# Performance work log

Hardware: AMD Instinct MI355X
Metric: run time of the kernel (lower is better)

Reference implementation:

```python
import jax, jax.numpy as jnp
import numpy as np

NUM_HEADS = 16
HEAD_DIM = 64
Q_DIM = K_DIM = V_DIM = 1024
LQ = LK = 4096
TAU = HEAD_DIM ** (-0.5)


def setup_inputs() -> dict:
    key = jax.random.key(0)
    ks = jax.random.split(key, 11)
    inner = NUM_HEADS * HEAD_DIM
    s = 0.02
    return {
        "q": jax.random.normal(ks[0], (LQ, Q_DIM), dtype=jnp.float32),
        "k": jax.random.normal(ks[1], (LK, K_DIM), dtype=jnp.float32),
        "v": jax.random.normal(ks[2], (LK, V_DIM), dtype=jnp.float32),
        "Wq": jax.random.normal(ks[3], (Q_DIM, inner), dtype=jnp.float32) * s,
        "bq": jax.random.normal(ks[4], (inner,), dtype=jnp.float32) * s,
        "Wk": jax.random.normal(ks[5], (K_DIM, inner), dtype=jnp.float32) * s,
        "bk": jax.random.normal(ks[6], (inner,), dtype=jnp.float32) * s,
        "Wv": jax.random.normal(ks[7], (V_DIM, inner), dtype=jnp.float32) * s,
        "bv": jax.random.normal(ks[8], (inner,), dtype=jnp.float32) * s,
        "Wo": jax.random.normal(ks[9], (inner, Q_DIM), dtype=jnp.float32) * s,
        "bo": jax.random.normal(ks[10], (Q_DIM,), dtype=jnp.float32) * s,
    }


def reference(q, k, v, Wq, bq, Wk, bk, Wv, bv, Wo, bo):
    h, x = NUM_HEADS, HEAD_DIM
    # projections: [L, h*x] -> per-head layout
    qh = (q @ Wq + bq).reshape(-1, h, x)  # [Lq, h, x]
    kh = (k @ Wk + bk).reshape(-1, h, x)  # [Lk, h, x]
    vh = (v @ Wv + bv).reshape(-1, h, x)  # [Lk, h, x]
    # scores: [h, Lq, Lk]
    att = jnp.einsum('qhx,khx->hqk', qh, kh) * TAU
    att = jax.nn.softmax(att, axis=-1)  # dropout=0.0 -> identity
    ctx = jnp.einsum('hqk,khx->qhx', att, vh).reshape(-1, h * x)  # [Lq, h*x]
    out = ctx @ Wo + bo  # [Lq, Q_DIM]
    return out, att
```

## Files before the change

kernel.cpp:

```cpp
#include <hip/hip_runtime.h>
#include <hip/hip_bf16.h>

typedef unsigned short ushort_t;
typedef __attribute__((ext_vector_type(8))) short short8;
typedef __attribute__((ext_vector_type(8))) __bf16 bf16x8;
typedef __attribute__((ext_vector_type(4))) float f32x4;

#define LQS 4096
#define LKS 4096
#define NH 16
#define HD 64
#define DIN 1024
#define QBLK 64
#define KVB 64
static constexpr float TAU_S = 0.125f;
static constexpr float LOG2E = 1.4426950408889634f;

__device__ __forceinline__ float exp2_fast(float x) { return __builtin_amdgcn_exp2f(x); }

__device__ __forceinline__ ushort_t f32_to_bf16(float x) {
  union { float f; unsigned u; } v; v.f = x;
  unsigned r = v.u + 0x7FFF + ((v.u >> 16) & 1);
  return (ushort_t)(r >> 16);
}

__device__ __forceinline__ void gld_lds16(const void* g, void* l) {
  __builtin_amdgcn_global_load_lds((const __attribute__((address_space(1))) void*)g,
                                   (__attribute__((address_space(3))) void*)l, 16, 0, 0);
}

__device__ __forceinline__ f32x4 mfma16(bf16x8 a, bf16x8 b, f32x4 c) {
  return __builtin_amdgcn_mfma_f32_16x16x32_bf16(a, b, c, 0, 0, 0);
}

struct Cvt3 { const float* src[3]; ushort_t* dst[3]; };
__global__ void cvt_kernel(Cvt3 c) {
  const float* __restrict__ src = c.src[blockIdx.y];
  ushort_t* __restrict__ dst = c.dst[blockIdx.y];
  int i = (blockIdx.x * 256 + threadIdx.x) * 8;
  float4 a = *(const float4*)(src + i);
  float4 b = *(const float4*)(src + i + 4);
  short8 o;
  o[0] = (short)f32_to_bf16(a.x); o[1] = (short)f32_to_bf16(a.y);
  o[2] = (short)f32_to_bf16(a.z); o[3] = (short)f32_to_bf16(a.w);
  o[4] = (short)f32_to_bf16(b.x); o[5] = (short)f32_to_bf16(b.y);
  o[6] = (short)f32_to_bf16(b.z); o[7] = (short)f32_to_bf16(b.w);
  *(short8*)(dst + i) = o;
}

struct TW4 { const float* W[4]; ushort_t* Wt[4]; };
__global__ void transpose_w(TW4 w) {
  const float* __restrict__ W = w.W[blockIdx.z];
  ushort_t* __restrict__ Wt = w.Wt[blockIdx.z];
  __shared__ float tile[64][65];
  const int t = threadIdx.x;
  const int k0 = blockIdx.y * 64, n0 = blockIdx.x * 64;
#pragma unroll
  for (int i = 0; i < 16; ++i) {
    int idx = i * 256 + t;
    int r = idx >> 6, c = idx & 63;
    tile[r][c] = W[(size_t)(k0 + r) * DIN + n0 + c];
  }
  __syncthreads();
#pragma unroll
  for (int i = 0; i < 16; ++i) {
    int idx = i * 256 + t;
    int r = idx >> 6, c = idx & 63;
    Wt[(size_t)(n0 + r) * DIN + k0 + c] = f32_to_bf16(tile[c][r]);
  }
}

__global__ void transpose_v(const ushort_t* __restrict__ vh, ushort_t* __restrict__ vt) {
  __shared__ ushort_t tile[64][65];
  const int t = threadIdx.x;
  const int k0 = blockIdx.x * 64, h = blockIdx.y;
#pragma unroll
  for (int i = 0; i < 16; ++i) {
    int idx = i * 256 + t;
    int r = idx >> 6, c = idx & 63;
    tile[r][c] = vh[(size_t)(k0 + r) * DIN + h * HD + c];
  }
  __syncthreads();
#pragma unroll
  for (int i = 0; i < 16; ++i) {
    int idx = i * 256 + t;
    int r = idx >> 6, c = idx & 63;
    vt[((size_t)h * HD + r) * (size_t)LKS + k0 + c] = tile[c][r];
  }
}

struct Batch3 {
  const ushort_t* A[3];
  const ushort_t* Bt[3];
  const float* bias[3];
  void* C[3];
  float scale[3];
};
template <bool OUT_F32>
__launch_bounds__(256, 2)
__global__ void gemm_nt(Batch3 bt3) {
  const int bid = blockIdx.x;
  const int xcd = bid & 7, idx = bid >> 3;
  const int z = idx >> 5, rem = idx & 31;
  const int by = xcd * 4 + (rem >> 3), bx = rem & 7;
  const ushort_t* __restrict__ A = bt3.A[z];
  const ushort_t* __restrict__ Bt = bt3.Bt[z];
  const float* __restrict__ bias = bt3.bias[z];
  void* __restrict__ Cout = bt3.C[z];
  const float scale = bt3.scale[z];
  const int K = DIN, N = DIN;

  __shared__ __align__(16) ushort_t Alds[128 * 64];
  __shared__ __align__(16) ushort_t Blds[128 * 64];
  const int t = threadIdx.x, wave = t >> 6, lane = t & 63;
  const int l15 = lane & 15, lg = lane >> 4;
  const int m0 = by * 128, n0 = bx * 128;
  const int wr = wave >> 1, wc = wave & 1;
  f32x4 acc[4][4];
#pragma unroll
  for (int i = 0; i < 4; ++i)
#pragma unroll
    for (int j = 0; j < 4; ++j) acc[i][j] = (f32x4){0.f, 0.f, 0.f, 0.f};

  for (int tk = 0; tk < K / 64; ++tk) {
#pragma unroll
    for (int c = 0; c < 4; ++c) {
      int chunk = wave * 4 + c;
      int row = chunk * 8 + (lane >> 3);
      int ss = (lane & 7) ^ (row & 7);
      gld_lds16(A + (size_t)(m0 + row) * K + tk * 64 + ss * 8, (char*)Alds + chunk * 1024);
      gld_lds16(Bt + (size_t)(n0 + row) * K + tk * 64 + ss * 8, (char*)Blds + chunk * 1024);
    }
    __syncthreads();
#pragma unroll
    for (int kk = 0; kk < 2; ++kk) {
      bf16x8 a[4], b[4];
#pragma unroll
      for (int i = 0; i < 4; ++i) {
        int ra = wr * 64 + i * 16 + l15;
        a[i] = *(const bf16x8*)((const char*)Alds + ra * 128 + ((((kk * 4 + lg) << 4)) ^ ((ra & 7) << 4)));
        int rb = wc * 64 + i * 16 + l15;
        b[i] = *(const bf16x8*)((const char*)Blds + rb * 128 + ((((kk * 4 + lg) << 4)) ^ ((rb & 7) << 4)));
      }
#pragma unroll
      for (int mi = 0; mi < 4; ++mi)
#pragma unroll
        for (int ni = 0; ni < 4; ++ni)
          acc[mi][ni] = mfma16(a[mi], b[ni], acc[mi][ni]);
    }
    __syncthreads();
  }
#pragma unroll
  for (int ni = 0; ni < 4; ++ni) {
    int coln = n0 + wc * 64 + ni * 16 + l15;
    float bv = bias[coln];
#pragma unroll
    for (int mi = 0; mi < 4; ++mi) {
#pragma unroll
      for (int r = 0; r < 4; ++r) {
        int rowm = m0 + wr * 64 + mi * 16 + lg * 4 + r;
        float v = (acc[mi][ni][r] + bv) * scale;
        if (OUT_F32)
          ((float*)Cout)[(size_t)rowm * N + coln] = v;
        else
          ((ushort_t*)Cout)[(size_t)rowm * N + coln] = f32_to_bf16(v);
      }
    }
  }
}

__launch_bounds__(256, 4)
__global__ void attn_kernel(const ushort_t* __restrict__ qh, const ushort_t* __restrict__ kh,
                            const ushort_t* __restrict__ vt, float* __restrict__ att,
                            ushort_t* __restrict__ ctx) {
  __shared__ __align__(16) ushort_t Klds[KVB * 64];
  __shared__ __align__(16) ushort_t Vlds[KVB * 64];
  __shared__ __align__(16) float Patt[4][16 * 64];
  const int t = threadIdx.x, wave = t >> 6, lane = t & 63;
  const int l15 = lane & 15, lg = lane >> 4;
  const int bid = blockIdx.x;
  const int xcd = bid & 7, idx = bid >> 3;
  const int h = xcd * 2 + (idx >> 6);
  const int q0 = (idx & 63) * QBLK;

  char* Pw = (char*)Patt[wave];

  bf16x8 qa[2];
  {
    int row = q0 + wave * 16 + l15;
    const ushort_t* qp = qh + (size_t)row * DIN + h * HD + lg * 8;
    qa[0] = *(const bf16x8*)(qp);
    qa[1] = *(const bf16x8*)(qp + 32);
  }

  const int srow8 = lane >> 3;
  const int sslot = (lane & 7);

  float rs[4] = {0.f, 0.f, 0.f, 0.f};
  for (int tk = 0; tk < LKS / KVB; ++tk) {
#pragma unroll
    for (int c = 0; c < 2; ++c) {
      int chunk = wave * 2 + c;
      int row = chunk * 8 + srow8;
      int ss = sslot ^ (row & 7);
      gld_lds16(kh + (size_t)(tk * KVB + row) * DIN + h * HD + ss * 8, (char*)Klds + chunk * 1024);
    }
    __syncthreads();
#pragma unroll
    for (int ct = 0; ct < 4; ++ct) {
      f32x4 acc = (f32x4){0.f, 0.f, 0.f, 0.f};
#pragma unroll
      for (int kk = 0; kk < 2; ++kk) {
        int row = ct * 16 + l15;
        bf16x8 kb = *(const bf16x8*)((const char*)Klds + row * 128 + ((((kk * 4 + lg) << 4)) ^ ((row & 7) << 4)));
        acc = mfma16(qa[kk], kb, acc);
      }
#pragma unroll
      for (int r = 0; r < 4; ++r) rs[r] += exp2_fast(acc[r]);
    }
    __syncthreads();
  }
#pragma unroll
  for (int m = 1; m < 16; m <<= 1) {
#pragma unroll
    for (int r = 0; r < 4; ++r) rs[r] += __shfl_xor(rs[r], m, 64);
  }
  float recip[4];
#pragma unroll
  for (int r = 0; r < 4; ++r) recip[r] = 1.0f / rs[r];

  f32x4 cacc[4];
#pragma unroll
  for (int x = 0; x < 4; ++x) cacc[x] = (f32x4){0.f, 0.f, 0.f, 0.f};
  float* atth = att + ((size_t)h << 24);

  for (int tk = 0; tk < LKS / KVB; ++tk) {
#pragma unroll
    for (int c = 0; c < 2; ++c) {
      int chunk = wave * 2 + c;
      int row = chunk * 8 + srow8;
      int ss = sslot ^ (row & 7);
      gld_lds16(kh + (size_t)(tk * KVB + row) * DIN + h * HD + ss * 8, (char*)Klds + chunk * 1024);
      gld_lds16(vt + ((size_t)h * HD + row) * (size_t)LKS + tk * KVB + ss * 8, (char*)Vlds + chunk * 1024);
    }
    __syncthreads();
#pragma unroll
    for (int ct = 0; ct < 4; ++ct) {
      f32x4 acc = (f32x4){0.f, 0.f, 0.f, 0.f};
#pragma unroll
      for (int kk = 0; kk < 2; ++kk) {
        int row = ct * 16 + l15;
        bf16x8 kb = *(const bf16x8*)((const char*)Klds + row * 128 + ((((kk * 4 + lg) << 4)) ^ ((row & 7) << 4)));
        acc = mfma16(qa[kk], kb, acc);
      }
#pragma unroll
      for (int r = 0; r < 4; ++r) {
        float p = exp2_fast(acc[r]) * recip[r];
        int R = lg * 4 + r;
        int col = ct * 16 + l15;
        int slot = col >> 2;
        *(float*)(Pw + R * 256 + (((slot ^ R)) << 4) + (col & 3) * 4) = p;
      }
    }
#pragma unroll
    for (int i = 0; i < 4; ++i) {
      int slot = lg + 4 * i;
      f32x4 v = *(const f32x4*)(Pw + l15 * 256 + ((slot ^ l15) << 4));
      int rowq = q0 + wave * 16 + l15;
      *(f32x4*)(atth + (((size_t)rowq) << 12) + tk * KVB + slot * 4) = v;
    }
    bf16x8 pa[2];
#pragma unroll
    for (int kk = 0; kk < 2; ++kk) {
      int s0 = kk * 8 + lg * 2;
      f32x4 lo = *(const f32x4*)(Pw + l15 * 256 + ((s0 ^ l15) << 4));
      f32x4 hi = *(const f32x4*)(Pw + l15 * 256 + (((s0 + 1) ^ l15) << 4));
      short8 sp;
#pragma unroll
      for (int j = 0; j < 4; ++j) {
        sp[j] = (short)f32_to_bf16(lo[j]);
        sp[4 + j] = (short)f32_to_bf16(hi[j]);
      }
      pa[kk] = *(bf16x8*)&sp;
    }
#pragma unroll
    for (int x = 0; x < 4; ++x) {
#pragma unroll
      for (int kk = 0; kk < 2; ++kk) {
        int rv = x * 16 + l15;
        bf16x8 vb = *(const bf16x8*)((const char*)Vlds + rv * 128 + ((((kk * 4 + lg) << 4)) ^ ((rv & 7) << 4)));
        cacc[x] = mfma16(pa[kk], vb, cacc[x]);
      }
    }
    __syncthreads();
  }
#pragma unroll
  for (int x = 0; x < 4; ++x) {
#pragma unroll
    for (int r = 0; r < 4; ++r) {
      int rowq = q0 + wave * 16 + lg * 4 + r;
      int col = h * HD + x * 16 + l15;
      ctx[(size_t)rowq * DIN + col] = f32_to_bf16(cacc[x][r]);
    }
  }
}

extern "C" void kernel_launch(void* const* d_in, const int* in_sizes, int n_in,
                              void* d_out, int out_size, void* d_ws, size_t ws_size,
                              hipStream_t stream) {
  const float* q = (const float*)d_in[0];
  const float* k = (const float*)d_in[1];
  const float* v = (const float*)d_in[2];
  const float* Wq = (const float*)d_in[3];
  const float* bq = (const float*)d_in[4];
  const float* Wk = (const float*)d_in[5];
  const float* bk = (const float*)d_in[6];
  const float* Wv = (const float*)d_in[7];
  const float* bv = (const float*)d_in[8];
  const float* Wo = (const float*)d_in[9];
  const float* bo = (const float*)d_in[10];

  float* out = (float*)d_out;
  float* att = out + (size_t)LQS * DIN;

  char* ws = (char*)d_ws;
  ushort_t* qhb = (ushort_t*)(ws + (size_t)0);
  ushort_t* khb = (ushort_t*)(ws + ((size_t)8 << 20));
  ushort_t* vhb = (ushort_t*)(ws + ((size_t)16 << 20));
  ushort_t* vtb = (ushort_t*)(ws + ((size_t)24 << 20));
  ushort_t* ctx = (ushort_t*)(ws + ((size_t)32 << 20));
  ushort_t* qb = (ushort_t*)(ws + ((size_t)40 << 20));
  ushort_t* kb = (ushort_t*)(ws + ((size_t)48 << 20));
  ushort_t* vb = (ushort_t*)(ws + ((size_t)56 << 20));
  ushort_t* Wqt = (ushort_t*)(ws + ((size_t)64 << 20));
  ushort_t* Wkt = (ushort_t*)(ws + ((size_t)66 << 20));
  ushort_t* Wvt = (ushort_t*)(ws + ((size_t)68 << 20));
  ushort_t* Wot = (ushort_t*)(ws + ((size_t)70 << 20));

  Cvt3 c3;
  c3.src[0] = q; c3.src[1] = k; c3.src[2] = v;
  c3.dst[0] = qb; c3.dst[1] = kb; c3.dst[2] = vb;
  cvt_kernel<<<dim3(LQS * DIN / 8 / 256, 3), 256, 0, stream>>>(c3);

  TW4 w4;
  w4.W[0] = Wq; w4.W[1] = Wk; w4.W[2] = Wv; w4.W[3] = Wo;
  w4.Wt[0] = Wqt; w4.Wt[1] = Wkt; w4.Wt[2] = Wvt; w4.Wt[3] = Wot;
  transpose_w<<<dim3(16, 16, 4), 256, 0, stream>>>(w4);

  Batch3 pb;
  pb.A[0] = qb; pb.A[1] = kb; pb.A[2] = vb;
  pb.Bt[0] = Wqt; pb.Bt[1] = Wkt; pb.Bt[2] = Wvt;
  pb.bias[0] = bq; pb.bias[1] = bk; pb.bias[2] = bv;
  pb.C[0] = qhb; pb.C[1] = khb; pb.C[2] = vhb;
  pb.scale[0] = TAU_S * LOG2E; pb.scale[1] = 1.0f; pb.scale[2] = 1.0f;
  gemm_nt<false><<<768, 256, 0, stream>>>(pb);

  transpose_v<<<dim3(64, 16), 256, 0, stream>>>(vhb, vtb);

  attn_kernel<<<1024, 256, 0, stream>>>(qhb, khb, vtb, att, ctx);

  Batch3 ob;
  ob.A[0] = ctx; ob.A[1] = ctx; ob.A[2] = ctx;
  ob.Bt[0] = Wot; ob.Bt[1] = Wot; ob.Bt[2] = Wot;
  ob.bias[0] = bo; ob.bias[1] = bo; ob.bias[2] = bo;
  ob.C[0] = out; ob.C[1] = out; ob.C[2] = out;
  ob.scale[0] = 1.0f; ob.scale[1] = 1.0f; ob.scale[2] = 1.0f;
  gemm_nt<true><<<256, 256, 0, stream>>>(ob);
}
```

Baseline: 451.9 us.

## Transpose QK^T MFMA to keep P in registers and drop LDS staging

Swaps the MFMA operand order so each lane holds a row of scores for one query, letting the probability tile be written to global memory and fed to the PV MFMA directly from registers instead of passing through an LDS staging buffer. The row-sum reduction is shortened to two shuffles, and normalization folds log2 of the sum into the exponent, removing a multiply per element. V operand fetches are rebuilt from two 8-byte LDS reads to match the new P register layout. This removes LDS write/read traffic for P and frees shared memory, but adds split V loads that may raise LDS instruction count.

After: 434.7 us. 1.04x faster.

```diff
diff --git a/kernel.cpp b/kernel.cpp
--- a/kernel.cpp
+++ b/kernel.cpp
@@ -17,6 +17,7 @@
 static constexpr float LOG2E = 1.4426950408889634f;
 
 __device__ __forceinline__ float exp2_fast(float x) { return __builtin_amdgcn_exp2f(x); }
+__device__ __forceinline__ float log2_fast(float x) { return __builtin_amdgcn_logf(x); }
 
 __device__ __forceinline__ ushort_t f32_to_bf16(float x) {
   union { float f; unsigned u; } v; v.f = x;
@@ -175,20 +176,17 @@
                             ushort_t* __restrict__ ctx) {
   __shared__ __align__(16) ushort_t Klds[KVB * 64];
   __shared__ __align__(16) ushort_t Vlds[KVB * 64];
-  __shared__ __align__(16) float Patt[4][16 * 64];
   const int t = threadIdx.x, wave = t >> 6, lane = t & 63;
   const int l15 = lane & 15, lg = lane >> 4;
   const int bid = blockIdx.x;
   const int xcd = bid & 7, idx = bid >> 3;
   const int h = xcd * 2 + (idx >> 6);
   const int q0 = (idx & 63) * QBLK;
-
-  char* Pw = (char*)Patt[wave];
+  const int w0 = q0 + wave * 16;
 
   bf16x8 qa[2];
   {
-    int row = q0 + wave * 16 + l15;
-    const ushort_t* qp = qh + (size_t)row * DIN + h * HD + lg * 8;
+    const ushort_t* qp = qh + (size_t)(w0 + l15) * DIN + h * HD + lg * 8;
     qa[0] = *(const bf16x8*)(qp);
     qa[1] = *(const bf16x8*)(qp + 32);
   }
@@ -196,7 +194,7 @@
   const int srow8 = lane >> 3;
   const int sslot = (lane & 7);
 
-  float rs[4] = {0.f, 0.f, 0.f, 0.f};
+  float rs_lane = 0.f;
   for (int tk = 0; tk < LKS / KVB; ++tk) {
 #pragma unroll
     for (int c = 0; c < 2; ++c) {
@@ -213,21 +211,16 @@
       for (int kk = 0; kk < 2; ++kk) {
         int row = ct * 16 + l15;
         bf16x8 kb = *(const bf16x8*)((const char*)Klds + row * 128 + ((((kk * 4 + lg) << 4)) ^ ((row & 7) << 4)));
-        acc = mfma16(qa[kk], kb, acc);
-      }
-#pragma unroll
-      for (int r = 0; r < 4; ++r) rs[r] += exp2_fast(acc[r]);
-    }
-    __syncthreads();
-  }
-#pragma unroll
-  for (int m = 1; m < 16; m <<= 1) {
-#pragma unroll
-    for (int r = 0; r < 4; ++r) rs[r] += __shfl_xor(rs[r], m, 64);
-  }
-  float recip[4];
-#pragma unroll
-  for (int r = 0; r < 4; ++r) recip[r] = 1.0f / rs[r];
+        acc = mfma16(kb, qa[kk], acc);
+      }
+#pragma unroll
+      for (int r = 0; r < 4; ++r) rs_lane += exp2_fast(acc[r]);
+    }
+    __syncthreads();
+  }
+  rs_lane += __shfl_xor(rs_lane, 16, 64);
+  rs_lane += __shfl_xor(rs_lane, 32, 64);
+  const float lrs = log2_fast(rs_lane);
 
   f32x4 cacc[4];
 #pragma unroll
@@ -244,6 +237,7 @@
       gld_lds16(vt + ((size_t)h * HD + row) * (size_t)LKS + tk * KVB + ss * 8, (char*)Vlds + chunk * 1024);
     }
     __syncthreads();
+    float p[4][4];
 #pragma unroll
     for (int ct = 0; ct < 4; ++ct) {
       f32x4 acc = (f32x4){0.f, 0.f, 0.f, 0.f};
@@ -251,45 +245,41 @@
       for (int kk = 0; kk < 2; ++kk) {
         int row = ct * 16 + l15;
         bf16x8 kb = *(const bf16x8*)((const char*)Klds + row * 128 + ((((kk * 4 + lg) << 4)) ^ ((row & 7) << 4)));
-        acc = mfma16(qa[kk], kb, acc);
-      }
-#pragma unroll
-      for (int r = 0; r < 4; ++r) {
-        float p = exp2_fast(acc[r]) * recip[r];
-        int R = lg * 4 + r;
-        int col = ct * 16 + l15;
-        int slot = col >> 2;
-        *(float*)(Pw + R * 256 + (((slot ^ R)) << 4) + (col & 3) * 4) = p;
-      }
-    }
-#pragma unroll
-    for (int i = 0; i < 4; ++i) {
-      int slot = lg + 4 * i;
-      f32x4 v = *(const f32x4*)(Pw + l15 * 256 + ((slot ^ l15) << 4));
-      int rowq = q0 + wave * 16 + l15;
-      *(f32x4*)(atth + (((size_t)rowq) << 12) + tk * KVB + slot * 4) = v;
+        acc = mfma16(kb, qa[kk], acc);
+      }
+#pragma unroll
+      for (int r = 0; r < 4; ++r) p[ct][r] = exp2_fast(acc[r] - lrs);
+    }
+#pragma unroll
+    for (int ct = 0; ct < 4; ++ct) {
+      f32x4 v = (f32x4){p[ct][0], p[ct][1], p[ct][2], p[ct][3]};
+      *(f32x4*)(atth + (((size_t)(w0 + l15)) << 12) + tk * KVB + ct * 16 + lg * 4) = v;
     }
     bf16x8 pa[2];
 #pragma unroll
     for (int kk = 0; kk < 2; ++kk) {
-      int s0 = kk * 8 + lg * 2;
-      f32x4 lo = *(const f32x4*)(Pw + l15 * 256 + ((s0 ^ l15) << 4));
-      f32x4 hi = *(const f32x4*)(Pw + l15 * 256 + (((s0 + 1) ^ l15) << 4));
       short8 sp;
 #pragma unroll
       for (int j = 0; j < 4; ++j) {
-        sp[j] = (short)f32_to_bf16(lo[j]);
-        sp[4 + j] = (short)f32_to_bf16(hi[j]);
+        sp[j] = (short)f32_to_bf16(p[2 * kk][j]);
+        sp[4 + j] = (short)f32_to_bf16(p[2 * kk + 1][j]);
       }
       pa[kk] = *(bf16x8*)&sp;
     }
 #pragma unroll
     for (int x = 0; x < 4; ++x) {
+      int row = x * 16 + l15;
+      const char* vrow = (const char*)Vlds + row * 128;
+      int par = row & 7;
+      int sub = (lg & 1) << 3;
 #pragma unroll
       for (int kk = 0; kk < 2; ++kk) {
-        int rv = x * 16 + l15;
-        bf16x8 vb = *(const bf16x8*)((const char*)Vlds + rv * 128 + ((((kk * 4 + lg) << 4)) ^ ((rv & 7) << 4)));
-        cacc[x] = mfma16(pa[kk], vb, cacc[x]);
+        int sA = (4 * kk + (lg >> 1)) ^ par;
+        int sB = (4 * kk + 2 + (lg >> 1)) ^ par;
+        union { unsigned long long q[2]; bf16x8 v; } U;
+        U.q[0] = *(const unsigned long long*)(vrow + (sA << 4) + sub);
+        U.q[1] = *(const unsigned long long*)(vrow + (sB << 4) + sub);
+        cacc[x] = mfma16(pa[kk], U.v, cacc[x]);
       }
     }
     __syncthreads();
@@ -298,7 +288,7 @@
   for (int x = 0; x < 4; ++x) {
 #pragma unroll
     for (int r = 0; r < 4; ++r) {
-      int rowq = q0 + wave * 16 + lg * 4 + r;
+      int rowq = w0 + lg * 4 + r;
       int col = h * HD + x * 16 + l15;
       ctx[(size_t)rowq * DIN + col] = f32_to_bf16(cacc[x][r]);
     }
```
